# Kernel optimization log

Hardware: AMD Instinct MI355X
Metric: run time of the kernel (lower is better)

## Reference

```python
import jax, jax.numpy as jnp
import numpy as np
from jax.scipy.special import gammaln

ALPHA = 1.0   # CRP concentration (init kwarg)
K_MAX = 64    # max number of clusters (z values are in [0, K_MAX))


def setup_inputs() -> dict:
    key = jax.random.key(0)
    k1, k2, k3, k4, k5, k6, k7 = jax.random.split(key, 7)
    B, T, D = 16, 1024, 256
    # Hurdle data: exact zeros with prob ~0.3, strictly positive otherwise
    mag = jax.random.uniform(k1, (B, T, D), dtype=jnp.float32) + 0.1
    keep = jax.random.uniform(k2, (B, T, D)) > 0.3
    X = jnp.where(keep, mag, 0.0)
    z = jax.random.randint(k3, (B, T), 0, K_MAX)
    loc = 0.1 * jax.random.normal(k4, (D,), dtype=jnp.float32)
    log_conc = 0.1 * jax.random.normal(k5, (D,), dtype=jnp.float32)
    log_scale = 0.1 * jax.random.normal(k6, (D,), dtype=jnp.float32)
    sparse_prior_logit = 0.1 * jax.random.normal(k7, (D,), dtype=jnp.float32)
    return {"X": X, "z": z, "loc": loc, "log_conc": log_conc,
            "log_scale": log_scale, "sparse_prior_logit": sparse_prior_logit}


def _loss(X, z, loc, log_conc, log_scale, sparse_prior_logit):
    B, T, D = X.shape
    conc = jnp.exp(log_conc)
    scale = jnp.exp(log_scale)
    # NIG prior on (mu, sigma^2) of log-values per dim
    m0 = loc                         # location
    kap0 = 2.0 * conc + 3.0          # mean concentration
    a0 = conc                        # IG shape
    b0 = scale                       # IG scale
    # Beta prior on the hurdle (success = nonzero observation)
    a1_0 = kap0 + 1.0                                  # concentration1
    a0_0 = (kap0 + 1.0) * jnp.exp(sparse_prior_logit)  # concentration0

    def bcast(v):  # [D] -> [B, K_MAX, D]
        return jnp.zeros((B, K_MAX, D), dtype=X.dtype) + v

    carry0 = (bcast(m0), bcast(kap0), bcast(a0), bcast(b0),
              bcast(a1_0), bcast(a0_0), jnp.zeros((B, K_MAX), dtype=X.dtype))

    bidx = jnp.arange(B)

    def step(carry, xs):
        m, kap, a, b, c1, c0, counts = carry
        x, k, t = xs                      # x [B,D], k [B], t scalar step index
        y = x > 0
        tl = jnp.log(jnp.where(y, x, 1.0))  # safe log of nonzero entries
        idx = (bidx, k)
        mk, kapk, ak, bk = m[idx], kap[idx], a[idx], b[idx]   # [B,D]
        c1k, c0k = c1[idx], c0[idx]
        ck = counts[idx]                                      # [B]
        # CRP sequential prior: count/(t+alpha) or alpha/(t+alpha) for new table
        crp = jnp.log(jnp.where(ck > 0, ck, ALPHA)) - jnp.log(t + ALPHA)
        # Beta-Bernoulli predictive for the hurdle indicator
        bern = jnp.where(y, jnp.log(c1k), jnp.log(c0k)) - jnp.log(c1k + c0k)
        # NIG posterior-predictive: Student-t on log x, plus -log x Jacobian
        nu = 2.0 * ak
        sig2 = bk * (kapk + 1.0) / (ak * kapk)
        zsq = (tl - mk) ** 2 / sig2
        lt = (gammaln(0.5 * (nu + 1.0)) - gammaln(0.5 * nu)
              - 0.5 * jnp.log(nu * jnp.pi) - 0.5 * jnp.log(sig2)
              - 0.5 * (nu + 1.0) * jnp.log1p(zsq / nu))
        cont = jnp.where(y, lt - tl, 0.0)
        lp = crp + (bern + cont).sum(-1)   # [B]
        # Conjugate sufficient-statistic updates for the chosen cluster
        m_n = jnp.where(y, (kapk * mk + tl) / (kapk + 1.0), mk)
        kap_n = jnp.where(y, kapk + 1.0, kapk)
        a_n = jnp.where(y, ak + 0.5, ak)
        b_n = jnp.where(y, bk + kapk * (tl - mk) ** 2 / (2.0 * (kapk + 1.0)), bk)
        c1_n = jnp.where(y, c1k + 1.0, c1k)
        c0_n = jnp.where(y, c0k, c0k + 1.0)
        carry = (m.at[idx].set(m_n), kap.at[idx].set(kap_n),
                 a.at[idx].set(a_n), b.at[idx].set(b_n),
                 c1.at[idx].set(c1_n), c0.at[idx].set(c0_n),
                 counts.at[idx].add(1.0))
        return carry, lp

    xs = (jnp.transpose(X, (1, 0, 2)), z.T, jnp.arange(T, dtype=X.dtype))
    _, lps = jax.lax.scan(step, carry0, xs)   # [T, B]
    trace_log_prob = lps.sum(0)               # [B]
    return (-trace_log_prob).mean()           # loss = nll_trace(X, z).mean()


def reference(X, z, loc, log_conc, log_scale, sparse_prior_logit):
    return _loss(X, z, loc, log_conc, log_scale, sparse_prior_logit)
```

## Files before the change

kernel.cpp:

```cpp
#include <hip/hip_runtime.h>
#include <math.h>

#define BB_ 16
#define TT_ 1024
#define DD_ 256
#define KK_ 64
#define ALPHA_ 1.0f

__global__ __launch_bounds__(256) void chains_kernel(
    const float* __restrict__ X,
    const int*   __restrict__ z,
    const float* __restrict__ loc,
    const float* __restrict__ log_conc,
    const float* __restrict__ log_scale,
    const float* __restrict__ spl,
    float* __restrict__ out) {
  const int bk = blockIdx.x;
  const int b  = bk >> 6;
  const int k  = bk & 63;
  const int d  = threadIdx.x;
  const int lane = d & 63;
  const int wave = d >> 6;

  __shared__ unsigned short tbuf[TT_];
  __shared__ int wsum[4];
  __shared__ float red[4];

  const int4 zv = *reinterpret_cast<const int4*>(z + b * TT_ + 4 * d);
  const int m0 = (zv.x == k), m1 = (zv.y == k), m2 = (zv.z == k), m3 = (zv.w == k);
  const int cnt = m0 + m1 + m2 + m3;

  int inc = cnt;
  #pragma unroll
  for (int off = 1; off < 64; off <<= 1) {
    int v = __shfl_up(inc, off, 64);
    if (lane >= off) inc += v;
  }
  if (lane == 63) wsum[wave] = inc;
  __syncthreads();
  int base = 0;
  #pragma unroll
  for (int w = 0; w < 4; ++w) if (w < wave) base += wsum[w];
  const int n = wsum[0] + wsum[1] + wsum[2] + wsum[3];

  int pos = base + inc - cnt;
  const int t0 = 4 * d;
  if (m0) tbuf[pos++] = (unsigned short)(t0    );
  if (m1) tbuf[pos++] = (unsigned short)(t0 + 1);
  if (m2) tbuf[pos++] = (unsigned short)(t0 + 2);
  if (m3) tbuf[pos++] = (unsigned short)(t0 + 3);
  __syncthreads();

  const float conc = __expf(log_conc[d]);
  float m    = loc[d];
  float kap  = 2.0f * conc + 3.0f;
  float a    = conc;
  float bb   = __expf(log_scale[d]);
  float c1   = kap + 1.0f;
  float c0   = c1 * __expf(spl[d]);
  float lgA  = lgammaf(a);
  float lgA5 = lgammaf(a + 0.5f);
  float acc  = 0.0f;

  const float LOG2PI = 1.837877066409345f;
  const float* Xb = X + (size_t)b * TT_ * DD_ + d;

  for (int j0 = 0; j0 < n; j0 += 4) {
    float xv[4];
    #pragma unroll
    for (int u = 0; u < 4; ++u) {
      xv[u] = (j0 + u < n) ? Xb[(size_t)tbuf[j0 + u] * DD_] : 0.0f;
    }
    #pragma unroll
    for (int u = 0; u < 4; ++u) {
      if (j0 + u < n) {
        const float x  = xv[u];
        const bool  y  = x > 0.0f;
        const float tl = y ? __logf(x) : 0.0f;

        const float bern = __logf(y ? c1 : c0) - __logf(c1 + c0);

        const float kap1   = kap + 1.0f;
        const float rk1    = __builtin_amdgcn_rcpf(kap1);
        const float la     = __logf(a);
        const float sig2   = bb * kap1 * __builtin_amdgcn_rcpf(a * kap);
        const float dm     = tl - m;
        const float zsq    = dm * dm * __builtin_amdgcn_rcpf(sig2);
        const float inv_2a = __builtin_amdgcn_rcpf(a + a);
        const float lt = (lgA5 - lgA)
                       - 0.5f * (LOG2PI + la)
                       - 0.5f * __logf(sig2)
                       - (a + 0.5f) * __logf(1.0f + zsq * inv_2a);

        acc += bern + (y ? (lt - tl) : 0.0f);

        const float bb_n   = bb + kap * dm * dm * 0.5f * rk1;
        const float m_n    = m + dm * rk1;
        const float lgA_n  = lgA5;
        const float lgA5_n = lgA + la;
        bb   = y ? bb_n   : bb;
        m    = y ? m_n    : m;
        lgA5 = y ? lgA5_n : lgA5;
        lgA  = y ? lgA_n  : lgA;
        kap  = y ? kap1      : kap;
        a    = y ? a + 0.5f  : a;
        c1   = y ? c1 + 1.0f : c1;
        c0   = y ? c0        : c0 + 1.0f;
      }
    }
  }

  for (int j = d; j < n; j += 256) {
    acc -= __logf((float)tbuf[j] + ALPHA_);
  }
  if (d == 0 && n > 0) {
    acc += lgammaf((float)n);
  }

  #pragma unroll
  for (int off = 32; off > 0; off >>= 1) acc += __shfl_down(acc, off, 64);
  if (lane == 0) red[wave] = acc;
  __syncthreads();
  if (d == 0) {
    const float s = red[0] + red[1] + red[2] + red[3];
    atomicAdd(out, -s * (1.0f / (float)BB_));
  }
}

extern "C" void kernel_launch(void* const* d_in, const int* in_sizes, int n_in,
                              void* d_out, int out_size, void* d_ws, size_t ws_size,
                              hipStream_t stream) {
  const float* X      = (const float*)d_in[0];
  const int*   z      = (const int*)  d_in[1];
  const float* loc    = (const float*)d_in[2];
  const float* lconc  = (const float*)d_in[3];
  const float* lscale = (const float*)d_in[4];
  const float* spl    = (const float*)d_in[5];
  float* out = (float*)d_out;

  hipMemsetAsync(out, 0, sizeof(float), stream);
  chains_kernel<<<BB_ * KK_, 256, 0, stream>>>(X, z, loc, lconc, lscale, spl, out);
}
```

Measured before the change: 93.20 us.

## Double-buffer X rows into LDS with async global-to-LDS loads

Each block's selected rows of X are now fetched in chunks of 8 rows into a double-buffered shared-memory tile using global_load_lds. Each wave issues 16-byte loads per lane. The first chunk is issued before the per-dimension prior setup and its lgamma calls, and each later chunk is prefetched while the current one is processed. This is meant to hide global load latency in the serial per-cluster recurrence, which before only prefetched four scalar loads at a time. The cost is an extra block barrier per chunk, 16 KB of LDS per block, and reliance on the barrier to wait for the async LDS writes.

```diff
diff --git a/kernel.cpp b/kernel.cpp
--- a/kernel.cpp
+++ b/kernel.cpp
@@ -6,6 +6,13 @@
 #define DD_ 256
 #define KK_ 64
 #define ALPHA_ 1.0f
+#define CH_ 8
+
+__device__ __forceinline__ void gl_lds16(const float* g, float* l) {
+  __builtin_amdgcn_global_load_lds(
+      (const __attribute__((address_space(1))) void*)g,
+      (__attribute__((address_space(3))) void*)l, 16, 0, 0);
+}
 
 __global__ __launch_bounds__(256) void chains_kernel(
     const float* __restrict__ X,
@@ -23,6 +30,7 @@
   const int wave = d >> 6;
 
   __shared__ unsigned short tbuf[TT_];
+  __shared__ float xs[2][CH_][DD_];
   __shared__ int wsum[4];
   __shared__ float red[4];
 
@@ -51,6 +59,23 @@
   if (m3) tbuf[pos++] = (unsigned short)(t0 + 3);
   __syncthreads();
 
+  const float* Xb = X + (size_t)b * TT_ * DD_;
+  const int nch = (n + CH_ - 1) / CH_;
+
+  #define ISSUE(c_, buf_)                                                \
+    do {                                                                 \
+      _Pragma("unroll")                                                  \
+      for (int rr = wave; rr < CH_; rr += 4) {                           \
+        const int j_ = (c_) * CH_ + rr;                                  \
+        if (j_ < n) {                                                    \
+          const int t_ = (int)tbuf[j_];                                  \
+          gl_lds16(Xb + (size_t)t_ * DD_ + lane * 4, &xs[buf_][rr][0]);  \
+        }                                                                \
+      }                                                                  \
+    } while (0)
+
+  if (nch > 0) ISSUE(0, 0);
+
   const float conc = __expf(log_conc[d]);
   float m    = loc[d];
   float kap  = 2.0f * conc + 3.0f;
@@ -63,51 +88,47 @@
   float acc  = 0.0f;
 
   const float LOG2PI = 1.837877066409345f;
-  const float* Xb = X + (size_t)b * TT_ * DD_ + d;
 
-  for (int j0 = 0; j0 < n; j0 += 4) {
-    float xv[4];
-    #pragma unroll
-    for (int u = 0; u < 4; ++u) {
-      xv[u] = (j0 + u < n) ? Xb[(size_t)tbuf[j0 + u] * DD_] : 0.0f;
+  int buf = 0;
+  for (int c = 0; c < nch; ++c) {
+    __syncthreads();
+    if (c + 1 < nch) ISSUE(c + 1, buf ^ 1);
+    const int jend = min(n - c * CH_, CH_);
+    for (int r = 0; r < jend; ++r) {
+      const float x  = xs[buf][r][d];
+      const bool  y  = x > 0.0f;
+      const float tl = y ? __logf(x) : 0.0f;
+
+      const float bern = __logf(y ? c1 : c0) - __logf(c1 + c0);
+
+      const float kap1   = kap + 1.0f;
+      const float rk1    = __builtin_amdgcn_rcpf(kap1);
+      const float la     = __logf(a);
+      const float sig2   = bb * kap1 * __builtin_amdgcn_rcpf(a * kap);
+      const float dm     = tl - m;
+      const float zsq    = dm * dm * __builtin_amdgcn_rcpf(sig2);
+      const float inv_2a = __builtin_amdgcn_rcpf(a + a);
+      const float lt = (lgA5 - lgA)
+                     - 0.5f * (LOG2PI + la)
+                     - 0.5f * __logf(sig2)
+                     - (a + 0.5f) * __logf(1.0f + zsq * inv_2a);
+
+      acc += bern + (y ? (lt - tl) : 0.0f);
+
+      const float bb_n   = bb + kap * dm * dm * 0.5f * rk1;
+      const float m_n    = m + dm * rk1;
+      const float lgA_n  = lgA5;
+      const float lgA5_n = lgA + la;
+      bb   = y ? bb_n   : bb;
+      m    = y ? m_n    : m;
+      lgA5 = y ? lgA5_n : lgA5;
+      lgA  = y ? lgA_n  : lgA;
+      kap  = y ? kap1      : kap;
+      a    = y ? a + 0.5f  : a;
+      c1   = y ? c1 + 1.0f : c1;
+      c0   = y ? c0        : c0 + 1.0f;
     }
-    #pragma unroll
-    for (int u = 0; u < 4; ++u) {
-      if (j0 + u < n) {
-        const float x  = xv[u];
-        const bool  y  = x > 0.0f;
-        const float tl = y ? __logf(x) : 0.0f;
-
-        const float bern = __logf(y ? c1 : c0) - __logf(c1 + c0);
-
-        const float kap1   = kap + 1.0f;
-        const float rk1    = __builtin_amdgcn_rcpf(kap1);
-        const float la     = __logf(a);
-        const float sig2   = bb * kap1 * __builtin_amdgcn_rcpf(a * kap);
-        const float dm     = tl - m;
-        const float zsq    = dm * dm * __builtin_amdgcn_rcpf(sig2);
-        const float inv_2a = __builtin_amdgcn_rcpf(a + a);
-        const float lt = (lgA5 - lgA)
-                       - 0.5f * (LOG2PI + la)
-                       - 0.5f * __logf(sig2)
-                       - (a + 0.5f) * __logf(1.0f + zsq * inv_2a);
-
-        acc += bern + (y ? (lt - tl) : 0.0f);
-
-        const float bb_n   = bb + kap * dm * dm * 0.5f * rk1;
-        const float m_n    = m + dm * rk1;
-        const float lgA_n  = lgA5;
-        const float lgA5_n = lgA + la;
-        bb   = y ? bb_n   : bb;
-        m    = y ? m_n    : m;
-        lgA5 = y ? lgA5_n : lgA5;
-        lgA  = y ? lgA_n  : lgA;
-        kap  = y ? kap1      : kap;
-        a    = y ? a + 0.5f  : a;
-        c1   = y ? c1 + 1.0f : c1;
-        c0   = y ? c0        : c0 + 1.0f;
-      }
-    }
+    buf ^= 1;
   }
 
   for (int j = d; j < n; j += 256) {
```

Result: no change. 92.85 us (-0.4%).
